# Kernel optimization log

Measured on AMD Instinct MI355X. Metric: run time of the kernel, lower is better.

## Reference

```python
import jax, jax.numpy as jnp
import numpy as np

WS = (4, 4, 4)      # window size (d, h, w)
SS = (2, 2, 2)      # shift size
NH = 12             # num heads
EPS = 1e-5


def _rel_pos_index(ws):
    # static numpy, identical to the torch buffer construction
    coords = np.stack(np.meshgrid(np.arange(ws[0]), np.arange(ws[1]), np.arange(ws[2]), indexing='ij'))
    cf = coords.reshape(3, -1)                       # (3, N)
    rc = cf[:, :, None] - cf[:, None, :]             # (3, N, N)
    rc = rc.transpose(1, 2, 0).astype(np.int64)      # (N, N, 3)
    rc[..., 0] += ws[0] - 1
    rc[..., 1] += ws[1] - 1
    rc[..., 2] += ws[2] - 1
    rc[..., 0] *= (2 * ws[1] - 1) * (2 * ws[2] - 1)
    rc[..., 1] *= 2 * ws[2] - 1
    return rc.sum(-1)                                # (N, N)


def _attn_mask(Dp, Hp, Wp, ws, ss):
    # static numpy mask for shifted windows: (nW, N, N), 0 or -100
    img = np.zeros((Dp, Hp, Wp))
    sl = lambda w, s: (slice(0, -w), slice(-w, -s), slice(-s, None))
    cnt = 0
    for d in sl(ws[0], ss[0]):
        for h in sl(ws[1], ss[1]):
            for w in sl(ws[2], ss[2]):
                img[d, h, w] = cnt
                cnt += 1
    m = img.reshape(Dp // ws[0], ws[0], Hp // ws[1], ws[1], Wp // ws[2], ws[2])
    m = m.transpose(0, 2, 4, 1, 3, 5).reshape(-1, ws[0] * ws[1] * ws[2])  # (nW, N)
    am = m[:, None, :] - m[:, :, None]
    return np.where(am != 0, -100.0, 0.0).astype(np.float32)


def _window_partition(x, ws):
    B, D, H, W, C = x.shape
    x = x.reshape(B, D // ws[0], ws[0], H // ws[1], ws[1], W // ws[2], ws[2], C)
    return x.transpose(0, 1, 3, 5, 2, 4, 6, 7).reshape(-1, ws[0] * ws[1] * ws[2], C)


def _window_reverse(win, ws, B, D, H, W):
    C = win.shape[-1]
    x = win.reshape(B, D // ws[0], H // ws[1], W // ws[2], ws[0], ws[1], ws[2], C)
    return x.transpose(0, 1, 4, 2, 5, 3, 6, 7).reshape(B, D, H, W, C)


def _layernorm(x, g, b):
    mu = jnp.mean(x, axis=-1, keepdims=True)
    var = jnp.mean(jnp.square(x - mu), axis=-1, keepdims=True)
    return (x - mu) * jax.lax.rsqrt(var + EPS) * g + b


def setup_inputs() -> dict:
    key = jax.random.key(0)
    ks = jax.random.split(key, 8)
    C, HID = 384, 1536
    s = 0.02
    return {
        'x': jax.random.normal(ks[0], (2, 16, 56, 56, C), jnp.float32),
        'norm1_g': jnp.ones((C,), jnp.float32),
        'norm1_b': jnp.zeros((C,), jnp.float32),
        'qkv_w': jax.random.normal(ks[1], (C, 3 * C), jnp.float32) * s,
        'qkv_b': jnp.zeros((3 * C,), jnp.float32),
        'rpb_table': jax.random.normal(ks[2], (343, NH), jnp.float32) * s,
        'proj_w': jax.random.normal(ks[3], (C, C), jnp.float32) * s,
        'proj_b': jnp.zeros((C,), jnp.float32),
        'norm2_g': jnp.ones((C,), jnp.float32),
        'norm2_b': jnp.zeros((C,), jnp.float32),
        'fc1_w': jax.random.normal(ks[4], (C, HID), jnp.float32) * s,
        'fc1_b': jnp.zeros((HID,), jnp.float32),
        'fc2_w': jax.random.normal(ks[5], (HID, C), jnp.float32) * s,
        'fc2_b': jnp.zeros((C,), jnp.float32),
    }


def reference(x, norm1_g, norm1_b, qkv_w, qkv_b, rpb_table, proj_w, proj_b,
              norm2_g, norm2_b, fc1_w, fc1_b, fc2_w, fc2_b):
    B, D, H, W, C = x.shape
    N = WS[0] * WS[1] * WS[2]
    hd = C // NH
    scale = hd ** -0.5

    shortcut = x
    h = _layernorm(x, norm1_g, norm1_b)
    # dims are divisible by window; pad amounts are zero (torch pad path is a no-op)
    Dp, Hp, Wp = D, H, W

    shifted = jnp.roll(h, shift=(-SS[0], -SS[1], -SS[2]), axis=(1, 2, 3))
    win = _window_partition(shifted, WS)                 # (B*nW, N, C)
    Bw = win.shape[0]
    nW = Bw // B

    qkv = (win @ qkv_w + qkv_b).reshape(Bw, N, 3, NH, hd)
    q, k, v = qkv[:, :, 0], qkv[:, :, 1], qkv[:, :, 2]   # (Bw, N, NH, hd)
    attn = jnp.einsum('bnhd,bmhd->bhnm', q * scale, k)   # (Bw, NH, N, N)

    rel_idx = jnp.asarray(_rel_pos_index(WS))            # (N, N) static
    bias = rpb_table[rel_idx.reshape(-1)].reshape(N, N, NH).transpose(2, 0, 1)
    attn = attn + bias[None]

    mask = jnp.asarray(_attn_mask(Dp, Hp, Wp, WS, SS))   # (nW, N, N) static
    attn = attn.reshape(B, nW, NH, N, N) + mask[None, :, None]
    attn = jax.nn.softmax(attn.reshape(Bw, NH, N, N), axis=-1)

    out = jnp.einsum('bhnm,bmhd->bnhd', attn, v).reshape(Bw, N, C)
    out = out @ proj_w + proj_b

    shifted = _window_reverse(out, WS, B, Dp, Hp, Wp)
    h = jnp.roll(shifted, shift=(SS[0], SS[1], SS[2]), axis=(1, 2, 3))

    x = shortcut + h
    h2 = _layernorm(x, norm2_g, norm2_b)
    h2 = jax.nn.gelu(h2 @ fc1_w + fc1_b, approximate=False) @ fc2_w + fc2_b
    return x + h2
```

## Files before the change

kernel.cpp:

```cpp
#include <hip/hip_runtime.h>
#include <math.h>

typedef unsigned short u16;
typedef float v4f __attribute__((ext_vector_type(4)));
typedef short v8s __attribute__((ext_vector_type(8)));

__device__ __forceinline__ u16 f2bf(float f) {
  union { float f; unsigned u; } c; c.f = f;
  unsigned u = c.u;
  u += 0x7fff + ((u >> 16) & 1);
  return (u16)(u >> 16);
}

__device__ __forceinline__ float fast_gelu(float x) {
  float t = x * x;
  float u = x * (2.3022082f + 0.10294325f * t);
  float e = __builtin_amdgcn_exp2f(-u);
  return x * __builtin_amdgcn_rcpf(1.f + e);
}

typedef __attribute__((address_space(1))) const unsigned int guint;
typedef __attribute__((address_space(3))) unsigned int luint;
__device__ __forceinline__ void gll16(const void* g, void* l) {
  __builtin_amdgcn_global_load_lds((guint*)g, (luint*)l, 16, 0, 0);
}

__device__ __forceinline__ int row_to_token(int r) {
  int win = r >> 6, n = r & 63;
  int b = (win >= 784) ? 1 : 0;
  int wrem = win - b * 784;
  int wd = wrem / 196;
  int r2 = wrem - wd * 196;
  int wh = r2 / 14;
  int ww = r2 - wh * 14;
  int d = wd * 4 + (n >> 4);
  int h = wh * 4 + ((n >> 2) & 3);
  int w = ww * 4 + (n & 3);
  d = (d + 2) & 15;
  h += 2; if (h >= 56) h -= 56;
  w += 2; if (w >= 56) w -= 56;
  return ((b * 16 + d) * 56 + h) * 56 + w;
}

__device__ __forceinline__ int region_label(int n, int bd, int bh, int bw) {
  int ld = bd ? (((n >> 4) >= 2) ? 2 : 1) : 0;
  int lh = bh ? ((((n >> 2) & 3) >= 2) ? 2 : 1) : 0;
  int lw = bw ? (((n & 3) >= 2) ? 2 : 1) : 0;
  return ld * 9 + lh * 3 + lw;
}

__global__ __launch_bounds__(256) void transpose_w(const float* __restrict__ src, u16* __restrict__ dst,
                                                   int K, int N) {
  __shared__ u16 t[32][33];
  int kt = blockIdx.x * 32, nt = blockIdx.y * 32;
  int lx = threadIdx.x & 31, ly = threadIdx.x >> 5;
#pragma unroll
  for (int i = 0; i < 32; i += 8)
    t[ly + i][lx] = f2bf(src[(size_t)(kt + ly + i) * N + nt + lx]);
  __syncthreads();
#pragma unroll
  for (int i = 0; i < 32; i += 8)
    dst[(size_t)(nt + ly + i) * K + kt + lx] = t[lx][ly + i];
}

__global__ __launch_bounds__(256) void bias_kernel(const float* __restrict__ rpb, float* __restrict__ biasb) {
  int i = blockIdx.x * 256 + threadIdx.x;
  int h = i >> 12, n = (i >> 6) & 63, m = i & 63;
  int dd = (n >> 4) - (m >> 4) + 3;
  int dh = ((n >> 2) & 3) - ((m >> 2) & 3) + 3;
  int dw = (n & 3) - (m & 3) + 3;
  biasb[i] = rpb[(dd * 49 + dh * 7 + dw) * 12 + h];
}

template<bool MAP>
__global__ __launch_bounds__(256) void ln_kernel(const float* __restrict__ x, const float* __restrict__ g,
                                                 const float* __restrict__ bta, u16* __restrict__ out) {
  int wid = threadIdx.x >> 6, lane = threadIdx.x & 63;
  int r = blockIdx.x * 4 + wid;
  int t = MAP ? row_to_token(r) : r;
  const float* src = x + (size_t)t * 384;
  float v[6]; float s = 0.f;
#pragma unroll
  for (int i = 0; i < 6; i++) { v[i] = src[lane + i * 64]; s += v[i]; }
#pragma unroll
  for (int off = 1; off < 64; off <<= 1) s += __shfl_xor(s, off);
  float mu = s * (1.f / 384.f);
  float vs = 0.f;
#pragma unroll
  for (int i = 0; i < 6; i++) { float d = v[i] - mu; vs += d * d; }
#pragma unroll
  for (int off = 1; off < 64; off <<= 1) vs += __shfl_xor(vs, off);
  float rstd = 1.f / sqrtf(vs * (1.f / 384.f) + 1e-5f);
  u16* dst = out + (size_t)r * 384;
#pragma unroll
  for (int i = 0; i < 6; i++) {
    int c = lane + i * 64;
    dst[c] = f2bf((v[i] - mu) * rstd * g[c] + bta[c]);
  }
}

template<int EPI>
__global__ __launch_bounds__(256) void gemm_bf16(const u16* __restrict__ A, const u16* __restrict__ Bw,
                                                 const float* __restrict__ bias, int N, int K,
                                                 u16* __restrict__ out_bf, float* __restrict__ out_f,
                                                 const float* __restrict__ resid, int ntn) {
  __shared__ __align__(16) u16 As[4096];
  __shared__ __align__(16) u16 Bs[4096];
  const int tid = threadIdx.x;
  const int nwg = gridDim.x;
  const int bid = blockIdx.x;
  const int swz = (bid & 7) * (nwg >> 3) + (bid >> 3);
  const int by = swz / ntn;
  const int bx = swz - by * ntn;
  const int m0 = by * 128, n0 = bx * 128;
  const int wid = tid >> 6, lane = tid & 63;
  const int wm = (wid >> 1) * 64, wn = (wid & 1) * 64;
  const int l15 = lane & 15, q4 = lane >> 4;

  const int u0 = tid, u1 = 256 + tid;
  const int r0 = u0 >> 2, r1 = u1 >> 2;
  const int c0 = ((u0 & 3) ^ ((r0 >> 1) & 3)) << 3;
  const int c1 = ((u1 & 3) ^ ((r1 >> 1) & 3)) << 3;
  const u16* ag0 = A + (size_t)(m0 + r0) * K + c0;
  const u16* ag1 = A + (size_t)(m0 + r1) * K + c1;
  const u16* bg0 = Bw + (size_t)(n0 + r0) * K + c0;
  const u16* bg1 = Bw + (size_t)(n0 + r1) * K + c1;
  u16* asd0 = As + (wid << 9);
  u16* asd1 = As + 2048 + (wid << 9);
  u16* bsd0 = Bs + (wid << 9);
  u16* bsd1 = Bs + 2048 + (wid << 9);

  int aoff[4], boff[4];
#pragma unroll
  for (int t = 0; t < 4; t++) {
    int ra = wm + t * 16 + l15;
    aoff[t] = ra * 64 + ((q4 ^ ((ra >> 1) & 3)) << 4);
    int rb = wn + t * 16 + l15;
    boff[t] = rb * 64 + ((q4 ^ ((rb >> 1) & 3)) << 4);
  }

  v4f acc[4][4];
#pragma unroll
  for (int i = 0; i < 4; i++)
#pragma unroll
    for (int j = 0; j < 4; j++) acc[i][j] = (v4f){0.f, 0.f, 0.f, 0.f};

  gll16(ag0, asd0); gll16(ag1, asd1);
  gll16(bg0, bsd0); gll16(bg1, bsd1);
  ag0 += 32; ag1 += 32; bg0 += 32; bg1 += 32;

  const int nk = K >> 5;
  for (int kk = 0; kk < nk; ++kk) {
    __syncthreads();
    v8s afr[4], bfr[4];
#pragma unroll
    for (int t = 0; t < 4; t++) {
      afr[t] = *(const v8s*)((const char*)As + aoff[t]);
      bfr[t] = *(const v8s*)((const char*)Bs + boff[t]);
    }
    __syncthreads();
    if (kk + 1 < nk) {
      gll16(ag0, asd0); gll16(ag1, asd1);
      gll16(bg0, bsd0); gll16(bg1, bsd1);
      ag0 += 32; ag1 += 32; bg0 += 32; bg1 += 32;
    }
#pragma unroll
    for (int tm = 0; tm < 4; tm++)
#pragma unroll
      for (int tn = 0; tn < 4; tn++)
        acc[tm][tn] = __builtin_amdgcn_mfma_f32_16x16x32_bf16(afr[tm], bfr[tn], acc[tm][tn], 0, 0, 0);
  }

  float bb[4]; int gc[4];
#pragma unroll
  for (int tn = 0; tn < 4; tn++) { gc[tn] = n0 + wn + tn * 16 + l15; bb[tn] = bias[gc[tn]]; }
#pragma unroll
  for (int tm = 0; tm < 4; tm++) {
#pragma unroll
    for (int r = 0; r < 4; r++) {
      const int grow = m0 + wm + tm * 16 + q4 * 4 + r;
      size_t rowbase;
      if constexpr (EPI == 1) rowbase = (size_t)row_to_token(grow) * 384;
      else rowbase = (size_t)grow * N;
#pragma unroll
      for (int tn = 0; tn < 4; tn++) {
        float val = acc[tm][tn][r] + bb[tn];
        if constexpr (EPI == 0) {
          out_bf[rowbase + gc[tn]] = f2bf(val);
        } else if constexpr (EPI == 2) {
          out_bf[rowbase + gc[tn]] = f2bf(fast_gelu(val));
        } else if constexpr (EPI == 1) {
          out_f[rowbase + gc[tn]] = resid[rowbase + gc[tn]] + val;
        } else {
          out_f[rowbase + gc[tn]] += val;
        }
      }
    }
  }
}

__global__ __launch_bounds__(256) void attn_kernel(const u16* __restrict__ qkv, const float* __restrict__ biasb,
                                                   u16* __restrict__ outb) {
  __shared__ u16 P[4][64][72];
  int wid = threadIdx.x >> 6, lane = threadIdx.x & 63;
  int g = blockIdx.x * 4 + wid;
  int win = g / 12, head = g - win * 12;
  int l15 = lane & 15, q4 = lane >> 4;
  const u16* base = qkv + (size_t)win * 64 * 1152;
  const u16* qp = base + head * 32;
  const u16* kp = base + 384 + head * 32;
  const u16* vp = base + 768 + head * 32;

  v8s a[4], kb[4];
#pragma unroll
  for (int tm = 0; tm < 4; tm++) a[tm] = *(const v8s*)(qp + (size_t)(tm * 16 + l15) * 1152 + q4 * 8);
#pragma unroll
  for (int tn = 0; tn < 4; tn++) kb[tn] = *(const v8s*)(kp + (size_t)(tn * 16 + l15) * 1152 + q4 * 8);
  v4f acc[4][4];
#pragma unroll
  for (int i = 0; i < 4; i++)
#pragma unroll
    for (int j = 0; j < 4; j++) acc[i][j] = (v4f){0.f, 0.f, 0.f, 0.f};
#pragma unroll
  for (int tm = 0; tm < 4; tm++)
#pragma unroll
    for (int tn = 0; tn < 4; tn++)
      acc[tm][tn] = __builtin_amdgcn_mfma_f32_16x16x32_bf16(a[tm], kb[tn], acc[tm][tn], 0, 0, 0);

  int wrem = win % 784;
  int wd = wrem / 196, r2 = wrem % 196, wh = r2 / 14, ww = r2 % 14;
  int bd = (wd == 3), bh = (wh == 13), bw = (ww == 13);
  const float* bptr = biasb + head * 4096;
  int mlab[4];
#pragma unroll
  for (int tn = 0; tn < 4; tn++) mlab[tn] = region_label(tn * 16 + l15, bd, bh, bw);

#pragma unroll
  for (int tm = 0; tm < 4; tm++) {
#pragma unroll
    for (int r = 0; r < 4; r++) {
      int n = tm * 16 + q4 * 4 + r;
      int nlab = region_label(n, bd, bh, bw);
      float sv[4];
      float mx = -1e30f;
#pragma unroll
      for (int tn = 0; tn < 4; tn++) {
        int m = tn * 16 + l15;
        float s = acc[tm][tn][r] * 0.17677669529663687f + bptr[n * 64 + m];
        if (mlab[tn] != nlab) s -= 100.f;
        sv[tn] = s;
        mx = fmaxf(mx, s);
      }
#pragma unroll
      for (int off = 1; off < 16; off <<= 1) mx = fmaxf(mx, __shfl_xor(mx, off));
      float sum = 0.f;
#pragma unroll
      for (int tn = 0; tn < 4; tn++) { float e = __expf(sv[tn] - mx); sv[tn] = e; sum += e; }
#pragma unroll
      for (int off = 1; off < 16; off <<= 1) sum += __shfl_xor(sum, off);
      float inv = 1.f / sum;
#pragma unroll
      for (int tn = 0; tn < 4; tn++) P[wid][n][tn * 16 + l15] = f2bf(sv[tn] * inv);
    }
  }
  __syncthreads();

  v4f o[4][2];
#pragma unroll
  for (int i = 0; i < 4; i++) { o[i][0] = (v4f){0.f,0.f,0.f,0.f}; o[i][1] = (v4f){0.f,0.f,0.f,0.f}; }
#pragma unroll
  for (int kt = 0; kt < 2; kt++) {
    v8s pa[4];
#pragma unroll
    for (int tm = 0; tm < 4; tm++) pa[tm] = *(const v8s*)&P[wid][tm * 16 + l15][kt * 32 + q4 * 8];
#pragma unroll
    for (int tn = 0; tn < 2; tn++) {
      v8s vb;
#pragma unroll
      for (int j = 0; j < 8; j++) vb[j] = (short)vp[(size_t)(kt * 32 + q4 * 8 + j) * 1152 + tn * 16 + l15];
#pragma unroll
      for (int tm = 0; tm < 4; tm++)
        o[tm][tn] = __builtin_amdgcn_mfma_f32_16x16x32_bf16(pa[tm], vb, o[tm][tn], 0, 0, 0);
    }
  }
#pragma unroll
  for (int tm = 0; tm < 4; tm++)
#pragma unroll
    for (int tn = 0; tn < 2; tn++)
#pragma unroll
      for (int r = 0; r < 4; r++) {
        int n = tm * 16 + q4 * 4 + r;
        outb[(size_t)(win * 64 + n) * 384 + head * 32 + tn * 16 + l15] = f2bf(o[tm][tn][r]);
      }
}

extern "C" void kernel_launch(void* const* d_in, const int* in_sizes, int n_in,
                              void* d_out, int out_size, void* d_ws, size_t ws_size,
                              hipStream_t stream) {
  const float* x      = (const float*)d_in[0];
  const float* n1g    = (const float*)d_in[1];
  const float* n1b    = (const float*)d_in[2];
  const float* qkv_w  = (const float*)d_in[3];
  const float* qkv_b  = (const float*)d_in[4];
  const float* rpb    = (const float*)d_in[5];
  const float* proj_w = (const float*)d_in[6];
  const float* proj_b = (const float*)d_in[7];
  const float* n2g    = (const float*)d_in[8];
  const float* n2b    = (const float*)d_in[9];
  const float* fc1_w  = (const float*)d_in[10];
  const float* fc1_b  = (const float*)d_in[11];
  const float* fc2_w  = (const float*)d_in[12];
  const float* fc2_b  = (const float*)d_in[13];
  float* out = (float*)d_out;
  char* ws = (char*)d_ws;

  u16*   wb    = (u16*)ws;
  float* biasb = (float*)(ws + 3538944);
  u16*   lnbuf = (u16*)(ws + 3735552);
  u16*   qkvb  = (u16*)(ws + 80805888);
  u16*   attnb = (u16*)(ws + 312016896);
  u16*   fc1ob = (u16*)(ws + 80805888);

  u16* qkv_wt  = wb;
  u16* proj_wt = wb + 442368;
  u16* fc1_wt  = wb + 589824;
  u16* fc2_wt  = wb + 1179648;

  transpose_w<<<dim3(12, 36), 256, 0, stream>>>(qkv_w,  qkv_wt,  384, 1152);
  transpose_w<<<dim3(12, 12), 256, 0, stream>>>(proj_w, proj_wt, 384, 384);
  transpose_w<<<dim3(12, 48), 256, 0, stream>>>(fc1_w,  fc1_wt,  384, 1536);
  transpose_w<<<dim3(48, 12), 256, 0, stream>>>(fc2_w,  fc2_wt,  1536, 384);
  bias_kernel<<<192, 256, 0, stream>>>(rpb, biasb);
  ln_kernel<true><<<25088, 256, 0, stream>>>(x, n1g, n1b, lnbuf);
  gemm_bf16<0><<<dim3(9 * 784), 256, 0, stream>>>(lnbuf, qkv_wt, qkv_b, 1152, 384, qkvb, nullptr, nullptr, 9);
  attn_kernel<<<4704, 256, 0, stream>>>(qkvb, biasb, attnb);
  gemm_bf16<1><<<dim3(3 * 784), 256, 0, stream>>>(attnb, proj_wt, proj_b, 384, 384, nullptr, out, x, 3);
  ln_kernel<false><<<25088, 256, 0, stream>>>(out, n2g, n2b, lnbuf);
  gemm_bf16<2><<<dim3(12 * 784), 256, 0, stream>>>(lnbuf, fc1_wt, fc1_b, 1536, 384, fc1ob, nullptr, nullptr, 12);
  gemm_bf16<3><<<dim3(3 * 784), 256, 0, stream>>>(fc1ob, fc2_wt, fc2_b, 384, 1536, nullptr, out, nullptr, 3);
}
```

Before: 1.083 ms.

## Double-buffer LDS tiles in bf16 GEMM to overlap global loads with MFMA

The GEMM's A/B shared-memory tiles become two-stage ping-pong buffers, and two K-tiles are prefetched up front. Each iteration waits only for the older tile (vmcnt(4)) before reading fragments. It then issues the load two steps ahead into the buffer it just consumed, with the final tile handled in a peeled tail. This hides global-to-LDS latency behind the MFMA work, which the single-buffer version fully exposed every K step. The cost is twice the LDS per block, which may reduce occupancy, plus hand-placed waitcnt and barriers that must stay correct.

```diff
diff --git a/kernel.cpp b/kernel.cpp
--- a/kernel.cpp
+++ b/kernel.cpp
@@ -104,8 +104,8 @@
                                                  const float* __restrict__ bias, int N, int K,
                                                  u16* __restrict__ out_bf, float* __restrict__ out_f,
                                                  const float* __restrict__ resid, int ntn) {
-  __shared__ __align__(16) u16 As[4096];
-  __shared__ __align__(16) u16 Bs[4096];
+  __shared__ __align__(16) u16 As[2][4096];
+  __shared__ __align__(16) u16 Bs[2][4096];
   const int tid = threadIdx.x;
   const int nwg = gridDim.x;
   const int bid = blockIdx.x;
@@ -125,10 +125,7 @@
   const u16* ag1 = A + (size_t)(m0 + r1) * K + c1;
   const u16* bg0 = Bw + (size_t)(n0 + r0) * K + c0;
   const u16* bg1 = Bw + (size_t)(n0 + r1) * K + c1;
-  u16* asd0 = As + (wid << 9);
-  u16* asd1 = As + 2048 + (wid << 9);
-  u16* bsd0 = Bs + (wid << 9);
-  u16* bsd1 = Bs + 2048 + (wid << 9);
+  const int wofs = wid << 9;
 
   int aoff[4], boff[4];
 #pragma unroll
@@ -145,24 +142,52 @@
 #pragma unroll
     for (int j = 0; j < 4; j++) acc[i][j] = (v4f){0.f, 0.f, 0.f, 0.f};
 
-  gll16(ag0, asd0); gll16(ag1, asd1);
-  gll16(bg0, bsd0); gll16(bg1, bsd1);
+  const int nk = K >> 5;
+
+  gll16(ag0, &As[0][wofs]); gll16(ag1, &As[0][2048 + wofs]);
+  gll16(bg0, &Bs[0][wofs]); gll16(bg1, &Bs[0][2048 + wofs]);
   ag0 += 32; ag1 += 32; bg0 += 32; bg1 += 32;
-
-  const int nk = K >> 5;
-  for (int kk = 0; kk < nk; ++kk) {
-    __syncthreads();
+  gll16(ag0, &As[1][wofs]); gll16(ag1, &As[1][2048 + wofs]);
+  gll16(bg0, &Bs[1][wofs]); gll16(bg1, &Bs[1][2048 + wofs]);
+  ag0 += 32; ag1 += 32; bg0 += 32; bg1 += 32;
+
+  for (int kk = 0; kk < nk - 1; ++kk) {
+    asm volatile("s_waitcnt vmcnt(4)" ::: "memory");
+    __builtin_amdgcn_s_barrier();
+    __builtin_amdgcn_sched_barrier(0);
+    const int b = kk & 1;
     v8s afr[4], bfr[4];
 #pragma unroll
     for (int t = 0; t < 4; t++) {
-      afr[t] = *(const v8s*)((const char*)As + aoff[t]);
-      bfr[t] = *(const v8s*)((const char*)Bs + boff[t]);
-    }
-    __syncthreads();
-    if (kk + 1 < nk) {
-      gll16(ag0, asd0); gll16(ag1, asd1);
-      gll16(bg0, bsd0); gll16(bg1, bsd1);
+      afr[t] = *(const v8s*)((const char*)&As[b][0] + aoff[t]);
+      bfr[t] = *(const v8s*)((const char*)&Bs[b][0] + boff[t]);
+    }
+    asm volatile("s_waitcnt lgkmcnt(0)" ::: "memory");
+    __builtin_amdgcn_sched_barrier(0);
+    __builtin_amdgcn_s_barrier();
+    __builtin_amdgcn_sched_barrier(0);
+    asm volatile("" ::: "memory");
+    if (kk + 2 < nk) {
+      gll16(ag0, &As[b][wofs]); gll16(ag1, &As[b][2048 + wofs]);
+      gll16(bg0, &Bs[b][wofs]); gll16(bg1, &Bs[b][2048 + wofs]);
       ag0 += 32; ag1 += 32; bg0 += 32; bg1 += 32;
+    }
+#pragma unroll
+    for (int tm = 0; tm < 4; tm++)
+#pragma unroll
+      for (int tn = 0; tn < 4; tn++)
+        acc[tm][tn] = __builtin_amdgcn_mfma_f32_16x16x32_bf16(afr[tm], bfr[tn], acc[tm][tn], 0, 0, 0);
+  }
+  {
+    asm volatile("s_waitcnt vmcnt(0)" ::: "memory");
+    __builtin_amdgcn_s_barrier();
+    __builtin_amdgcn_sched_barrier(0);
+    const int b = (nk - 1) & 1;
+    v8s afr[4], bfr[4];
+#pragma unroll
+    for (int t = 0; t < 4; t++) {
+      afr[t] = *(const v8s*)((const char*)&As[b][0] + aoff[t]);
+      bfr[t] = *(const v8s*)((const char*)&Bs[b][0] + boff[t]);
     }
 #pragma unroll
     for (int tm = 0; tm < 4; tm++)
```

New measurement: 1.082 ms. Within noise of the previous version (-0.1%).

## Load GEMM fragments directly from global memory, dropping LDS staging

Applied to the files above, without the earlier changes.

Removes the shared-memory tiles and direct-to-LDS loads from the bf16 GEMM, so each wave reads its MFMA operand fragments straight from global memory through the cache, with no barriers. It also sets launch bounds to 4 blocks per CU to raise occupancy. This removes the two barriers per k-step and the LDS traffic, but every wave now fetches its A and B fragments separately. That replication, plus strided 16-byte row reads, leans heavily on L1/L2 and may cost more than the LDS path saved.

```diff
diff --git a/kernel.cpp b/kernel.cpp
--- a/kernel.cpp
+++ b/kernel.cpp
@@ -17,12 +17,6 @@
   float u = x * (2.3022082f + 0.10294325f * t);
   float e = __builtin_amdgcn_exp2f(-u);
   return x * __builtin_amdgcn_rcpf(1.f + e);
-}
-
-typedef __attribute__((address_space(1))) const unsigned int guint;
-typedef __attribute__((address_space(3))) unsigned int luint;
-__device__ __forceinline__ void gll16(const void* g, void* l) {
-  __builtin_amdgcn_global_load_lds((guint*)g, (luint*)l, 16, 0, 0);
 }
 
 __device__ __forceinline__ int row_to_token(int r) {
@@ -100,12 +94,10 @@
 }
 
 template<int EPI>
-__global__ __launch_bounds__(256) void gemm_bf16(const u16* __restrict__ A, const u16* __restrict__ Bw,
-                                                 const float* __restrict__ bias, int N, int K,
-                                                 u16* __restrict__ out_bf, float* __restrict__ out_f,
-                                                 const float* __restrict__ resid, int ntn) {
-  __shared__ __align__(16) u16 As[4096];
-  __shared__ __align__(16) u16 Bs[4096];
+__global__ __launch_bounds__(256, 4) void gemm_bf16(const u16* __restrict__ A, const u16* __restrict__ Bw,
+                                                    const float* __restrict__ bias, int N, int K,
+                                                    u16* __restrict__ out_bf, float* __restrict__ out_f,
+                                                    const float* __restrict__ resid, int ntn) {
   const int tid = threadIdx.x;
   const int nwg = gridDim.x;
   const int bid = blockIdx.x;
@@ -117,26 +109,12 @@
   const int wm = (wid >> 1) * 64, wn = (wid & 1) * 64;
   const int l15 = lane & 15, q4 = lane >> 4;
 
-  const int u0 = tid, u1 = 256 + tid;
-  const int r0 = u0 >> 2, r1 = u1 >> 2;
-  const int c0 = ((u0 & 3) ^ ((r0 >> 1) & 3)) << 3;
-  const int c1 = ((u1 & 3) ^ ((r1 >> 1) & 3)) << 3;
-  const u16* ag0 = A + (size_t)(m0 + r0) * K + c0;
-  const u16* ag1 = A + (size_t)(m0 + r1) * K + c1;
-  const u16* bg0 = Bw + (size_t)(n0 + r0) * K + c0;
-  const u16* bg1 = Bw + (size_t)(n0 + r1) * K + c1;
-  u16* asd0 = As + (wid << 9);
-  u16* asd1 = As + 2048 + (wid << 9);
-  u16* bsd0 = Bs + (wid << 9);
-  u16* bsd1 = Bs + 2048 + (wid << 9);
-
-  int aoff[4], boff[4];
+  const u16* ap[4];
+  const u16* bp[4];
 #pragma unroll
   for (int t = 0; t < 4; t++) {
-    int ra = wm + t * 16 + l15;
-    aoff[t] = ra * 64 + ((q4 ^ ((ra >> 1) & 3)) << 4);
-    int rb = wn + t * 16 + l15;
-    boff[t] = rb * 64 + ((q4 ^ ((rb >> 1) & 3)) << 4);
+    ap[t] = A  + (size_t)(m0 + wm + t * 16 + l15) * K + q4 * 8;
+    bp[t] = Bw + (size_t)(n0 + wn + t * 16 + l15) * K + q4 * 8;
   }
 
   v4f acc[4][4];
@@ -145,30 +123,19 @@
 #pragma unroll
     for (int j = 0; j < 4; j++) acc[i][j] = (v4f){0.f, 0.f, 0.f, 0.f};
 
-  gll16(ag0, asd0); gll16(ag1, asd1);
-  gll16(bg0, bsd0); gll16(bg1, bsd1);
-  ag0 += 32; ag1 += 32; bg0 += 32; bg1 += 32;
-
-  const int nk = K >> 5;
-  for (int kk = 0; kk < nk; ++kk) {
-    __syncthreads();
-    v8s afr[4], bfr[4];
+#pragma unroll 2
+  for (int k = 0; k < K; k += 32) {
+    v8s af[4], bf_[4];
 #pragma unroll
     for (int t = 0; t < 4; t++) {
-      afr[t] = *(const v8s*)((const char*)As + aoff[t]);
-      bfr[t] = *(const v8s*)((const char*)Bs + boff[t]);
+      af[t]  = *(const v8s*)(ap[t] + k);
+      bf_[t] = *(const v8s*)(bp[t] + k);
     }
-    __syncthreads();
-    if (kk + 1 < nk) {
-      gll16(ag0, asd0); gll16(ag1, asd1);
-      gll16(bg0, bsd0); gll16(bg1, bsd1);
-      ag0 += 32; ag1 += 32; bg0 += 32; bg1 += 32;
-    }
 #pragma unroll
     for (int tm = 0; tm < 4; tm++)
 #pragma unroll
       for (int tn = 0; tn < 4; tn++)
-        acc[tm][tn] = __builtin_amdgcn_mfma_f32_16x16x32_bf16(afr[tm], bfr[tn], acc[tm][tn], 0, 0, 0);
+        acc[tm][tn] = __builtin_amdgcn_mfma_f32_16x16x32_bf16(af[tm], bf_[tn], acc[tm][tn], 0, 0, 0);
   }
 
   float bb[4]; int gc[4];
```

Result: slower. 1.923 ms (+77.6%).
